# Kernel tuning notes

Measured on AMD Instinct MI355X. Metric: run time of the kernel, lower is better.

Reference implementation:

```python
import jax, jax.numpy as jnp
import numpy as np

NUM_HEADS = 16
HIDDEN = 1024
DIM = HIDDEN // NUM_HEADS  # 64
NEG = -1e8
LN_EPS = 1e-5


def setup_inputs() -> dict:
    key = jax.random.key(0)
    ks = jax.random.split(key, 8)
    B, Lq, Lk = 8, 512, 2048
    s = 0.02
    return {
        "input_embed": jax.random.normal(ks[0], (B, Lq, HIDDEN), jnp.float32),
        "kg_embed": jax.random.normal(ks[1], (B, Lk, HIDDEN), jnp.float32),
        "input_mask": jnp.ones((B, Lq), jnp.float32),
        "kg_mask": jnp.ones((B, Lk), jnp.float32),
        "Wq": jax.random.normal(ks[2], (DIM, DIM), jnp.float32) * s,
        "Wk": jax.random.normal(ks[3], (DIM, DIM), jnp.float32) * s,
        "Wv": jax.random.normal(ks[4], (DIM, DIM), jnp.float32) * s,
        "W_lin": jax.random.normal(ks[5], (HIDDEN, HIDDEN), jnp.float32) * s,
        "b_lin": jnp.zeros((HIDDEN,), jnp.float32),
        "ln_gamma": jnp.ones((HIDDEN,), jnp.float32),
        "ln_beta": jnp.zeros((HIDDEN,), jnp.float32),
    }


def reference(input_embed, kg_embed, input_mask, kg_mask, Wq, Wk, Wv, W_lin, b_lin, ln_gamma, ln_beta):
    B, Lq, H = input_embed.shape
    Lk = kg_embed.shape[1]
    # split heads: per-head slices share the SAME dim x dim q/k/v weights
    xq = input_embed.reshape(B, Lq, NUM_HEADS, DIM)
    xk = kg_embed.reshape(B, Lk, NUM_HEADS, DIM)
    q = jnp.einsum('bqhd,ed->bqhe', xq, Wq)  # Linear: x @ W.T
    k = jnp.einsum('bkhd,ed->bkhe', xk, Wk)
    v = jnp.einsum('bkhd,ed->bkhe', xk, Wv)
    scores = jnp.einsum('bqhd,bkhd->bhqk', q, k) / np.sqrt(DIM)  # [B,H,Lq,Lk]
    # additive masks: query-side and key-side
    scores = scores + ((1.0 - input_mask) * NEG)[:, None, :, None] \
                    + ((1.0 - kg_mask) * NEG)[:, None, None, :]
    attn = jax.nn.softmax(scores, axis=-1)
    ctx = jnp.einsum('bhqk,bkhd->bqhd', attn, v).reshape(B, Lq, H)  # concat heads
    lin = ctx @ W_lin.T + b_lin
    x = jax.nn.gelu(lin, approximate=False) + input_embed  # nn.GELU() is exact erf
    mu = jnp.mean(x, axis=-1, keepdims=True)
    var = jnp.mean(jnp.square(x - mu), axis=-1, keepdims=True)
    return (x - mu) * jax.lax.rsqrt(var + LN_EPS) * ln_gamma + ln_beta
```

## Files before the change

kernel.cpp:

```cpp
#include <hip/hip_runtime.h>
#include <cstdint>

#define BATCH 8
#define LQ 512
#define LK 2048
#define NH 16
#define DIM 64
#define HID 1024
#define NTOK (BATCH * LQ)
#define NKT (LK / 64)
#define KP 72
#define SC 0.1803368801111204f
#define NEGM (-1.4426950408889634e8f)

typedef _Float16 f16x8 __attribute__((ext_vector_type(8)));
typedef __fp16 half2v __attribute__((ext_vector_type(2)));
typedef float f32x4 __attribute__((ext_vector_type(4)));

#define MFMA(a, b, c) __builtin_amdgcn_mfma_f32_16x16x32_f16((a), (b), (c), 0, 0, 0)

__device__ __forceinline__ f16x8 ld8(const _Float16* p) { return *(const f16x8*)p; }

__device__ __forceinline__ void gl_lds16(const void* g, void* l) {
  __builtin_amdgcn_global_load_lds(
      (const __attribute__((address_space(1))) uint32_t*)g,
      (__attribute__((address_space(3))) uint32_t*)l, 16, 0, 0);
}

__device__ __forceinline__ void lds_barrier() {
  asm volatile("s_waitcnt lgkmcnt(0)" ::: "memory");
  __builtin_amdgcn_s_barrier();
}

__device__ __forceinline__ f16x8 cvt8(const float* p) {
  const float4 a = *(const float4*)p;
  const float4 b = *(const float4*)(p + 4);
  f16x8 v;
  v[0] = (_Float16)a.x; v[1] = (_Float16)a.y; v[2] = (_Float16)a.z; v[3] = (_Float16)a.w;
  v[4] = (_Float16)b.x; v[5] = (_Float16)b.y; v[6] = (_Float16)b.z; v[7] = (_Float16)b.w;
  return v;
}

__device__ __forceinline__ uint2 pk4(float a, float b, float c, float d) {
  union { half2v h2[2]; uint2 u; } t;
  t.h2[0] = __builtin_amdgcn_cvt_pkrtz(a, b);
  t.h2[1] = __builtin_amdgcn_cvt_pkrtz(c, d);
  return t.u;
}

__device__ __forceinline__ f16x8 pk8(float4 a, float4 b) {
  union { half2v h2[4]; f16x8 v; } t;
  t.h2[0] = __builtin_amdgcn_cvt_pkrtz(a.x, a.y);
  t.h2[1] = __builtin_amdgcn_cvt_pkrtz(a.z, a.w);
  t.h2[2] = __builtin_amdgcn_cvt_pkrtz(b.x, b.y);
  t.h2[3] = __builtin_amdgcn_cvt_pkrtz(b.z, b.w);
  return t.v;
}

__global__ __launch_bounds__(512, 2) void attn_kernel(
    const float* __restrict__ Xq, const float* __restrict__ Xk,
    const float* __restrict__ Wq, const float* __restrict__ Wk,
    const float* __restrict__ Wv, const float* __restrict__ kg_mask,
    _Float16* __restrict__ ctx) {
  __shared__ __align__(16) _Float16 Kl[2][64 * KP];
  __shared__ __align__(16) _Float16 Vl[2][64 * KP];
  __shared__ __align__(16) _Float16 Pl[8][2][16 * KP];
  const int tid = threadIdx.x;
  const int wave = tid >> 6, lane = tid & 63, l16 = lane & 15, quad = lane >> 4;
  const int kw = wave & 3;
  const int b = blockIdx.x >> 4, h = blockIdx.x & 15;
  const int qbase = blockIdx.y * 256;
  const float* Xg = Xk + (size_t)b * LK * HID + h * 64;
  const float* mg = kg_mask + (size_t)b * LK;

  const float* xrow0 = Xg + (size_t)(kw * 16 + l16) * HID + quad * 8;
  float4 xf0, xf1, xf2, xf3;
  auto loadX = [&](int kt) {
    const float* xr = xrow0 + (size_t)kt * HID;
    xf0 = *(const float4*)(xr);
    xf1 = *(const float4*)(xr + 4);
    xf2 = *(const float4*)(xr + 32);
    xf3 = *(const float4*)(xr + 36);
  };
  loadX(0);

  f16x8 aq0[2], aq1[2];
  {
    f16x8 wq0[4], wq1[4];
#pragma unroll
    for (int nt = 0; nt < 4; ++nt) {
      const float* wp = Wq + (nt * 16 + l16) * DIM + quad * 8;
      wq0[nt] = cvt8(wp);
      wq1[nt] = cvt8(wp + 32);
    }
#pragma unroll
    for (int qt = 0; qt < 2; ++qt) {
      const int qg = qbase + wave * 32 + qt * 16 + l16;
      const float* xpq = Xq + (size_t)(b * LQ + qg) * HID + h * 64 + quad * 8;
      const f16x8 bq0 = cvt8(xpq), bq1 = cvt8(xpq + 32);
#pragma unroll
      for (int nt = 0; nt < 4; ++nt) {
        f32x4 d = {0.f, 0.f, 0.f, 0.f};
        d = MFMA(wq0[nt], bq0, d);
        d = MFMA(wq1[nt], bq1, d);
        *(uint2*)&Pl[wave][qt][l16 * KP + nt * 16 + quad * 4] =
            pk4(d[0] * SC, d[1] * SC, d[2] * SC, d[3] * SC);
      }
      aq0[qt] = ld8(&Pl[wave][qt][l16 * KP + quad * 8]);
      aq1[qt] = ld8(&Pl[wave][qt][l16 * KP + 32 + quad * 8]);
    }
  }

  const float* Wsel = (wave < 4) ? Wk : Wv;
  f16x8 aw0[4], aw1[4];
#pragma unroll
  for (int nt = 0; nt < 4; ++nt) {
    const float* wp = Wsel + (nt * 16 + l16) * DIM + quad * 8;
    aw0[nt] = cvt8(wp);
    aw1[nt] = cvt8(wp + 32);
  }

  const f32x4 z4 = {0.f, 0.f, 0.f, 0.f};

  {
    const f16x8 bx0 = pk8(xf0, xf1), bx1 = pk8(xf2, xf3);
    if (wave < 4) {
#pragma unroll
      for (int nt = 0; nt < 4; ++nt) {
        f32x4 d = z4;
        d = MFMA(aw0[nt], bx0, d);
        d = MFMA(aw1[nt], bx1, d);
        *(uint2*)&Kl[0][(kw * 16 + l16) * KP + nt * 16 + quad * 4] =
            pk4(d[0], d[1], d[2], d[3]);
      }
    } else {
#pragma unroll
      for (int dt = 0; dt < 4; ++dt) {
        f32x4 d = z4;
        d = MFMA(bx0, aw0[dt], d);
        d = MFMA(bx1, aw1[dt], d);
        *(uint2*)&Vl[0][(dt * 16 + l16) * KP + kw * 16 + quad * 4] =
            pk4(d[0], d[1], d[2], d[3]);
      }
    }
  }
  loadX(64);
  lds_barrier();

  f32x4 o[2][4];
  float l_run[2] = {0.f, 0.f};
#pragma unroll
  for (int qt = 0; qt < 2; ++qt)
#pragma unroll
    for (int i = 0; i < 4; ++i) o[qt][i] = z4;

  for (int t = 0; t < NKT; ++t) {
    const int buf = t & 1;
    const int kt = t * 64;

    float4 mq[4];
#pragma unroll
    for (int nt = 0; nt < 4; ++nt)
      mq[nt] = *(const float4*)(mg + kt + nt * 16 + quad * 4);

    if (t + 1 < NKT) {
      const f16x8 bx0 = pk8(xf0, xf1), bx1 = pk8(xf2, xf3);
      if (wave < 4) {
#pragma unroll
        for (int nt = 0; nt < 4; ++nt) {
          f32x4 d = z4;
          d = MFMA(aw0[nt], bx0, d);
          d = MFMA(aw1[nt], bx1, d);
          *(uint2*)&Kl[buf ^ 1][(kw * 16 + l16) * KP + nt * 16 + quad * 4] =
              pk4(d[0], d[1], d[2], d[3]);
        }
      } else {
#pragma unroll
        for (int dt = 0; dt < 4; ++dt) {
          f32x4 d = z4;
          d = MFMA(bx0, aw0[dt], d);
          d = MFMA(bx1, aw1[dt], d);
          *(uint2*)&Vl[buf ^ 1][(dt * 16 + l16) * KP + kw * 16 + quad * 4] =
              pk4(d[0], d[1], d[2], d[3]);
        }
      }
      if (t + 2 < NKT) loadX(kt + 128);
    }

    f32x4 cin[4];
#pragma unroll
    for (int nt = 0; nt < 4; ++nt) {
      cin[nt][0] = __builtin_fmaf(mq[nt].x, -NEGM, NEGM);
      cin[nt][1] = __builtin_fmaf(mq[nt].y, -NEGM, NEGM);
      cin[nt][2] = __builtin_fmaf(mq[nt].z, -NEGM, NEGM);
      cin[nt][3] = __builtin_fmaf(mq[nt].w, -NEGM, NEGM);
    }

    float p[2][4][4];
    __builtin_amdgcn_s_setprio(1);
#pragma unroll
    for (int nt = 0; nt < 4; ++nt) {
      const f16x8 kb0 = ld8(&Kl[buf][(nt * 16 + l16) * KP + quad * 8]);
      const f16x8 kb1 = ld8(&Kl[buf][(nt * 16 + l16) * KP + 32 + quad * 8]);
#pragma unroll
      for (int qt = 0; qt < 2; ++qt) {
        f32x4 s = cin[nt];
        s = MFMA(kb0, aq0[qt], s);
        s = MFMA(kb1, aq1[qt], s);
        const float e0 = __builtin_amdgcn_exp2f(s[0]);
        const float e1 = __builtin_amdgcn_exp2f(s[1]);
        const float e2 = __builtin_amdgcn_exp2f(s[2]);
        const float e3 = __builtin_amdgcn_exp2f(s[3]);
        l_run[qt] += (e0 + e1) + (e2 + e3);
        p[qt][nt][0] = e0; p[qt][nt][1] = e1; p[qt][nt][2] = e2; p[qt][nt][3] = e3;
      }
    }
    __builtin_amdgcn_s_setprio(0);

#pragma unroll
    for (int qt = 0; qt < 2; ++qt)
#pragma unroll
      for (int nt = 0; nt < 4; ++nt)
        *(uint2*)&Pl[wave][qt][l16 * KP + nt * 16 + quad * 4] =
            pk4(p[qt][nt][0], p[qt][nt][1], p[qt][nt][2], p[qt][nt][3]);
    f16x8 ap0[2], ap1[2];
#pragma unroll
    for (int qt = 0; qt < 2; ++qt) {
      ap0[qt] = ld8(&Pl[wave][qt][l16 * KP + quad * 8]);
      ap1[qt] = ld8(&Pl[wave][qt][l16 * KP + 32 + quad * 8]);
    }

    __builtin_amdgcn_s_setprio(1);
#pragma unroll
    for (int dt = 0; dt < 4; ++dt) {
      const f16x8 vb0 = ld8(&Vl[buf][(dt * 16 + l16) * KP + quad * 8]);
      const f16x8 vb1 = ld8(&Vl[buf][(dt * 16 + l16) * KP + 32 + quad * 8]);
#pragma unroll
      for (int qt = 0; qt < 2; ++qt) {
        o[qt][dt] = MFMA(vb0, ap0[qt], o[qt][dt]);
        o[qt][dt] = MFMA(vb1, ap1[qt], o[qt][dt]);
      }
    }
    __builtin_amdgcn_s_setprio(0);

    lds_barrier();
  }

  float inv[2];
#pragma unroll
  for (int qt = 0; qt < 2; ++qt) {
    float s = l_run[qt];
    s += __shfl_xor(s, 16);
    s += __shfl_xor(s, 32);
    inv[qt] = 1.f / s;
  }
#pragma unroll
  for (int qt = 0; qt < 2; ++qt) {
    const int qg = qbase + wave * 32 + qt * 16 + l16;
    _Float16* base = ctx + (size_t)(b * LQ + qg) * HID + h * 64;
#pragma unroll
    for (int dt = 0; dt < 4; ++dt)
      *(uint2*)(base + dt * 16 + quad * 4) =
          pk4(o[qt][dt][0] * inv[qt], o[qt][dt][1] * inv[qt],
              o[qt][dt][2] * inv[qt], o[qt][dt][3] * inv[qt]);
  }
}

__global__ __launch_bounds__(256) void wconv_kernel(const float* __restrict__ W,
                                                    _Float16* __restrict__ Wh) {
  const int i = blockIdx.x * 256 + threadIdx.x;
  const float4 v = ((const float4*)W)[i];
  ((uint2*)Wh)[i] = pk4(v.x, v.y, v.z, v.w);
}

__global__ __launch_bounds__(512) void linear_kernel(const _Float16* __restrict__ A,
                                                     const _Float16* __restrict__ Wh,
                                                     const float* __restrict__ bias,
                                                     const float* __restrict__ resid,
                                                     float* __restrict__ Xout) {
  __shared__ __align__(16) _Float16 Al[2][128 * 64];
  __shared__ __align__(16) _Float16 Bl[2][128 * 64];
  const int tid = threadIdx.x;
  const int wave = tid >> 6, lane = tid & 63, l16 = lane & 15, quad = lane >> 4;
  const int wm = wave >> 2, wn = wave & 3;
  const int nbase = blockIdx.x * 128, mbase = blockIdx.y * 128;
  const int srow = wave * 16 + (lane >> 3);
  const int sc = lane & 7;

  auto stage = [&](int kk, int nbuf) {
#pragma unroll
    for (int i = 0; i < 2; ++i) {
      const int row = srow + i * 8;
      const int c = sc ^ (row & 7);
      gl_lds16(A + (size_t)(mbase + row) * HID + kk + c * 8,
               &Al[nbuf][(wave * 16 + i * 8) * 64]);
      gl_lds16(Wh + (size_t)(nbase + row) * HID + kk + c * 8,
               &Bl[nbuf][(wave * 16 + i * 8) * 64]);
    }
  };

  const f32x4 z4 = {0.f, 0.f, 0.f, 0.f};
  f32x4 acc[4][2];
#pragma unroll
  for (int mt = 0; mt < 4; ++mt)
#pragma unroll
    for (int nt = 0; nt < 2; ++nt) acc[mt][nt] = z4;

  stage(0, 0);
  for (int t = 0; t < HID / 64; ++t) {
    const int buf = t & 1;
    __syncthreads();
    if (t + 1 < HID / 64) stage((t + 1) * 64, buf ^ 1);
    const int sw = l16 & 7;
    f16x8 b0[2], b1[2];
#pragma unroll
    for (int nt = 0; nt < 2; ++nt) {
      const int brow = wn * 32 + nt * 16 + l16;
      b0[nt] = ld8(&Bl[buf][brow * 64 + (quad ^ sw) * 8]);
      b1[nt] = ld8(&Bl[buf][brow * 64 + ((quad + 4) ^ sw) * 8]);
    }
#pragma unroll
    for (int mt = 0; mt < 4; ++mt) {
      const int arow = wm * 64 + mt * 16 + l16;
      const f16x8 a0 = ld8(&Al[buf][arow * 64 + (quad ^ sw) * 8]);
      const f16x8 a1 = ld8(&Al[buf][arow * 64 + ((quad + 4) ^ sw) * 8]);
#pragma unroll
      for (int nt = 0; nt < 2; ++nt) {
        acc[mt][nt] = MFMA(a0, b0[nt], acc[mt][nt]);
        acc[mt][nt] = MFMA(a1, b1[nt], acc[mt][nt]);
      }
    }
  }
#pragma unroll
  for (int nt = 0; nt < 2; ++nt) {
    const int col = nbase + wn * 32 + nt * 16 + l16;
    const float bv = bias[col];
#pragma unroll
    for (int mt = 0; mt < 4; ++mt) {
#pragma unroll
      for (int r = 0; r < 4; ++r) {
        const int row = mbase + wm * 64 + mt * 16 + quad * 4 + r;
        const float v = acc[mt][nt][r] + bv;
        const float g = 0.5f * v * (1.f + erff(v * 0.70710678118654752f));
        Xout[(size_t)row * HID + col] = g + resid[(size_t)row * HID + col];
      }
    }
  }
}

__global__ __launch_bounds__(256) void ln_kernel(const float* __restrict__ X,
                                                 const float* __restrict__ gamma,
                                                 const float* __restrict__ beta,
                                                 float* __restrict__ out) {
  const int row = blockIdx.x, tid = threadIdx.x;
  const int lane = tid & 63, wave = tid >> 6;
  const float4 v = *(const float4*)(X + (size_t)row * HID + tid * 4);
  float s1 = v.x + v.y + v.z + v.w;
  float s2 = v.x * v.x + v.y * v.y + v.z * v.z + v.w * v.w;
#pragma unroll
  for (int off = 1; off < 64; off <<= 1) {
    s1 += __shfl_xor(s1, off);
    s2 += __shfl_xor(s2, off);
  }
  __shared__ float r1[4], r2[4];
  if (lane == 0) { r1[wave] = s1; r2[wave] = s2; }
  __syncthreads();
  s1 = r1[0] + r1[1] + r1[2] + r1[3];
  s2 = r2[0] + r2[1] + r2[2] + r2[3];
  const float mu = s1 * (1.f / HID);
  const float var = s2 * (1.f / HID) - mu * mu;
  const float rstd = rsqrtf(var + 1e-5f);
  const float4 g = *(const float4*)(gamma + tid * 4);
  const float4 be = *(const float4*)(beta + tid * 4);
  float4 ov;
  ov.x = (v.x - mu) * rstd * g.x + be.x;
  ov.y = (v.y - mu) * rstd * g.y + be.y;
  ov.z = (v.z - mu) * rstd * g.z + be.z;
  ov.w = (v.w - mu) * rstd * g.w + be.w;
  *(float4*)(out + (size_t)row * HID + tid * 4) = ov;
}

extern "C" void kernel_launch(void* const* d_in, const int* in_sizes, int n_in,
                              void* d_out, int out_size, void* d_ws, size_t ws_size,
                              hipStream_t stream) {
  (void)in_sizes; (void)n_in; (void)out_size; (void)ws_size;
  const float* input_embed = (const float*)d_in[0];
  const float* kg_embed    = (const float*)d_in[1];
  const float* kg_mask = (const float*)d_in[3];
  const float* Wq    = (const float*)d_in[4];
  const float* Wk    = (const float*)d_in[5];
  const float* Wv    = (const float*)d_in[6];
  const float* W_lin = (const float*)d_in[7];
  const float* b_lin = (const float*)d_in[8];
  const float* gamma = (const float*)d_in[9];
  const float* beta  = (const float*)d_in[10];

  char* ws = (char*)d_ws;
  _Float16* ctx = (_Float16*)(ws);
  float*    Xb  = (float*)(ws + (8u << 20));
  _Float16* Wh  = (_Float16*)(ws + (24u << 20));

  attn_kernel<<<dim3(128, 2), dim3(512), 0, stream>>>(input_embed, kg_embed, Wq, Wk, Wv,
                                                      kg_mask, ctx);
  wconv_kernel<<<dim3(1024), dim3(256), 0, stream>>>(W_lin, Wh);
  linear_kernel<<<dim3(8, 32), dim3(512), 0, stream>>>(ctx, Wh, b_lin, input_embed, Xb);
  ln_kernel<<<dim3(NTOK), dim3(256), 0, stream>>>(Xb, gamma, beta, (float*)d_out);
}
```

Measured before the change: 210.7 us.

## Split attention over key dimension with partial outputs and combine kernel

Splits the key/value sequence into two halves across a new grid z dimension, so the attention kernel launches twice as many blocks. Each split writes unnormalized fp32 partial outputs and row sums, and a new combine kernel sums them, normalizes and emits fp16 context. This works without max-rescaling because the softmax has no running max. The aim is to fill the MI355X's CUs better than the original 256-block grid did. The cost is recomputing the Q projection per split, extra global traffic for the fp32 partials, and one more kernel launch. It also shrinks the P scratch LDS buffer to one tile per wave.

```diff
diff --git a/kernel.cpp b/kernel.cpp
--- a/kernel.cpp
+++ b/kernel.cpp
@@ -57,19 +57,23 @@
   return t.v;
 }
 
+template <int NZ>
 __global__ __launch_bounds__(512, 2) void attn_kernel(
     const float* __restrict__ Xq, const float* __restrict__ Xk,
     const float* __restrict__ Wq, const float* __restrict__ Wk,
     const float* __restrict__ Wv, const float* __restrict__ kg_mask,
-    _Float16* __restrict__ ctx) {
+    _Float16* __restrict__ ctx, float* __restrict__ Opart,
+    float* __restrict__ lpart) {
   __shared__ __align__(16) _Float16 Kl[2][64 * KP];
   __shared__ __align__(16) _Float16 Vl[2][64 * KP];
-  __shared__ __align__(16) _Float16 Pl[8][2][16 * KP];
+  __shared__ __align__(16) _Float16 Pl[8][16 * KP];
   const int tid = threadIdx.x;
   const int wave = tid >> 6, lane = tid & 63, l16 = lane & 15, quad = lane >> 4;
   const int kw = wave & 3;
   const int b = blockIdx.x >> 4, h = blockIdx.x & 15;
   const int qbase = blockIdx.y * 256;
+  const int kz = blockIdx.z * (LK / NZ);
+  const int NT = NKT / NZ;
   const float* Xg = Xk + (size_t)b * LK * HID + h * 64;
   const float* mg = kg_mask + (size_t)b * LK;
 
@@ -82,7 +86,7 @@
     xf2 = *(const float4*)(xr + 32);
     xf3 = *(const float4*)(xr + 36);
   };
-  loadX(0);
+  loadX(kz);
 
   f16x8 aq0[2], aq1[2];
   {
@@ -103,11 +107,11 @@
         f32x4 d = {0.f, 0.f, 0.f, 0.f};
         d = MFMA(wq0[nt], bq0, d);
         d = MFMA(wq1[nt], bq1, d);
-        *(uint2*)&Pl[wave][qt][l16 * KP + nt * 16 + quad * 4] =
+        *(uint2*)&Pl[wave][l16 * KP + nt * 16 + quad * 4] =
             pk4(d[0] * SC, d[1] * SC, d[2] * SC, d[3] * SC);
       }
-      aq0[qt] = ld8(&Pl[wave][qt][l16 * KP + quad * 8]);
-      aq1[qt] = ld8(&Pl[wave][qt][l16 * KP + 32 + quad * 8]);
+      aq0[qt] = ld8(&Pl[wave][l16 * KP + quad * 8]);
+      aq1[qt] = ld8(&Pl[wave][l16 * KP + 32 + quad * 8]);
     }
   }
 
@@ -144,7 +148,7 @@
       }
     }
   }
-  loadX(64);
+  loadX(kz + 64);
   lds_barrier();
 
   f32x4 o[2][4];
@@ -154,16 +158,16 @@
 #pragma unroll
     for (int i = 0; i < 4; ++i) o[qt][i] = z4;
 
-  for (int t = 0; t < NKT; ++t) {
+  for (int t = 0; t < NT; ++t) {
     const int buf = t & 1;
-    const int kt = t * 64;
+    const int kt = kz + t * 64;
 
     float4 mq[4];
 #pragma unroll
     for (int nt = 0; nt < 4; ++nt)
       mq[nt] = *(const float4*)(mg + kt + nt * 16 + quad * 4);
 
-    if (t + 1 < NKT) {
+    if (t + 1 < NT) {
       const f16x8 bx0 = pk8(xf0, xf1), bx1 = pk8(xf2, xf3);
       if (wave < 4) {
 #pragma unroll
@@ -184,7 +188,7 @@
               pk4(d[0], d[1], d[2], d[3]);
         }
       }
-      if (t + 2 < NKT) loadX(kt + 128);
+      if (t + 2 < NT) loadX(kt + 128);
     }
 
     f32x4 cin[4];
@@ -217,17 +221,15 @@
     }
     __builtin_amdgcn_s_setprio(0);
 
-#pragma unroll
-    for (int qt = 0; qt < 2; ++qt)
+    f16x8 ap0[2], ap1[2];
+#pragma unroll
+    for (int qt = 0; qt < 2; ++qt) {
 #pragma unroll
       for (int nt = 0; nt < 4; ++nt)
-        *(uint2*)&Pl[wave][qt][l16 * KP + nt * 16 + quad * 4] =
+        *(uint2*)&Pl[wave][l16 * KP + nt * 16 + quad * 4] =
             pk4(p[qt][nt][0], p[qt][nt][1], p[qt][nt][2], p[qt][nt][3]);
-    f16x8 ap0[2], ap1[2];
-#pragma unroll
-    for (int qt = 0; qt < 2; ++qt) {
-      ap0[qt] = ld8(&Pl[wave][qt][l16 * KP + quad * 8]);
-      ap1[qt] = ld8(&Pl[wave][qt][l16 * KP + 32 + quad * 8]);
+      ap0[qt] = ld8(&Pl[wave][l16 * KP + quad * 8]);
+      ap1[qt] = ld8(&Pl[wave][l16 * KP + 32 + quad * 8]);
     }
 
     __builtin_amdgcn_s_setprio(1);
@@ -246,24 +248,50 @@
     lds_barrier();
   }
 
-  float inv[2];
 #pragma unroll
   for (int qt = 0; qt < 2; ++qt) {
     float s = l_run[qt];
     s += __shfl_xor(s, 16);
     s += __shfl_xor(s, 32);
-    inv[qt] = 1.f / s;
-  }
-#pragma unroll
-  for (int qt = 0; qt < 2; ++qt) {
     const int qg = qbase + wave * 32 + qt * 16 + l16;
-    _Float16* base = ctx + (size_t)(b * LQ + qg) * HID + h * 64;
-#pragma unroll
-    for (int dt = 0; dt < 4; ++dt)
-      *(uint2*)(base + dt * 16 + quad * 4) =
-          pk4(o[qt][dt][0] * inv[qt], o[qt][dt][1] * inv[qt],
-              o[qt][dt][2] * inv[qt], o[qt][dt][3] * inv[qt]);
-  }
+    if constexpr (NZ == 1) {
+      const float inv = 1.f / s;
+      _Float16* base = ctx + (size_t)(b * LQ + qg) * HID + h * 64;
+#pragma unroll
+      for (int dt = 0; dt < 4; ++dt)
+        *(uint2*)(base + dt * 16 + quad * 4) =
+            pk4(o[qt][dt][0] * inv, o[qt][dt][1] * inv,
+                o[qt][dt][2] * inv, o[qt][dt][3] * inv);
+    } else {
+      if (quad == 0)
+        lpart[((size_t)(blockIdx.z * BATCH + b) * NH + h) * LQ + qg] = s;
+      float* obase = Opart + (size_t)blockIdx.z * NTOK * HID +
+                     (size_t)(b * LQ + qg) * HID + h * 64;
+#pragma unroll
+      for (int dt = 0; dt < 4; ++dt) {
+        float4 ov;
+        ov.x = o[qt][dt][0]; ov.y = o[qt][dt][1];
+        ov.z = o[qt][dt][2]; ov.w = o[qt][dt][3];
+        *(float4*)(obase + dt * 16 + quad * 4) = ov;
+      }
+    }
+  }
+}
+
+__global__ __launch_bounds__(256) void combine_kernel(
+    const float* __restrict__ Opart, const float* __restrict__ lpart,
+    _Float16* __restrict__ ctx) {
+  const int tok = blockIdx.x, t = threadIdx.x;
+  const int b = tok >> 9, q = tok & 511;
+  const int hh = t >> 4;
+  const float l0 = lpart[((size_t)b * NH + hh) * LQ + q];
+  const float l1 = lpart[((size_t)(BATCH + b) * NH + hh) * LQ + q];
+  const float inv = 1.f / (l0 + l1);
+  const size_t off = (size_t)tok * HID + t * 4;
+  const float4 a = *(const float4*)(Opart + off);
+  const float4 c = *(const float4*)(Opart + (size_t)NTOK * HID + off);
+  *(uint2*)(ctx + off) = pk4((a.x + c.x) * inv, (a.y + c.y) * inv,
+                             (a.z + c.z) * inv, (a.w + c.w) * inv);
 }
 
 __global__ __launch_bounds__(256) void wconv_kernel(const float* __restrict__ W,
@@ -383,7 +411,7 @@
 extern "C" void kernel_launch(void* const* d_in, const int* in_sizes, int n_in,
                               void* d_out, int out_size, void* d_ws, size_t ws_size,
                               hipStream_t stream) {
-  (void)in_sizes; (void)n_in; (void)out_size; (void)ws_size;
+  (void)in_sizes; (void)n_in; (void)out_size;
   const float* input_embed = (const float*)d_in[0];
   const float* kg_embed    = (const float*)d_in[1];
   const float* kg_mask = (const float*)d_in[3];
@@ -399,9 +427,17 @@
   _Float16* ctx = (_Float16*)(ws);
   float*    Xb  = (float*)(ws + (8u << 20));
   _Float16* Wh  = (_Float16*)(ws + (24u << 20));
-
-  attn_kernel<<<dim3(128, 2), dim3(512), 0, stream>>>(input_embed, kg_embed, Wq, Wk, Wv,
-                                                      kg_mask, ctx);
+  float* Opart  = (float*)(ws + (26u << 20));
+  float* lpart  = (float*)(ws + (58u << 20));
+
+  if (ws_size >= (59ull << 20)) {
+    attn_kernel<2><<<dim3(128, 2, 2), dim3(512), 0, stream>>>(
+        input_embed, kg_embed, Wq, Wk, Wv, kg_mask, ctx, Opart, lpart);
+    combine_kernel<<<dim3(NTOK), dim3(256), 0, stream>>>(Opart, lpart, ctx);
+  } else {
+    attn_kernel<1><<<dim3(128, 2, 1), dim3(512), 0, stream>>>(
+        input_embed, kg_embed, Wq, Wk, Wv, kg_mask, ctx, Opart, lpart);
+  }
   wconv_kernel<<<dim3(1024), dim3(256), 0, stream>>>(W_lin, Wh);
   linear_kernel<<<dim3(8, 32), dim3(512), 0, stream>>>(ctx, Wh, b_lin, input_embed, Xb);
   ln_kernel<<<dim3(NTOK), dim3(256), 0, stream>>>(Xb, gamma, beta, (float*)d_out);
```

New measurement: 229.7 us. +9.0%, slower.

## Switch attention to 32x32x16 MFMA and pass P via permlane32 swap

Applied to the files above, without the earlier changes.

Rewrites the attention inner loop to use 32x32x16 f16 MFMA tiles instead of 16x16x32, giving each wave a single 32-query tile with 32x32 score and output accumulators. The probability matrix is re-laid out into the B-operand format in registers with permlane32_swap, replacing the LDS store and reload through Pl. This is meant to cut LDS traffic and MFMA instruction count per tile. In exchange it uses more accumulator registers and changes the mask and output indexing, which risks register pressure and occupancy at 2 blocks per CU.

```diff
diff --git a/kernel.cpp b/kernel.cpp
--- a/kernel.cpp
+++ b/kernel.cpp
@@ -16,8 +16,11 @@
 typedef _Float16 f16x8 __attribute__((ext_vector_type(8)));
 typedef __fp16 half2v __attribute__((ext_vector_type(2)));
 typedef float f32x4 __attribute__((ext_vector_type(4)));
+typedef float f32x16 __attribute__((ext_vector_type(16)));
+typedef unsigned uint2v __attribute__((ext_vector_type(2)));
 
 #define MFMA(a, b, c) __builtin_amdgcn_mfma_f32_16x16x32_f16((a), (b), (c), 0, 0, 0)
+#define MFMA32(a, b, c) __builtin_amdgcn_mfma_f32_32x32x16_f16((a), (b), (c), 0, 0, 0)
 
 __device__ __forceinline__ f16x8 ld8(const _Float16* p) { return *(const f16x8*)p; }
 
@@ -45,6 +48,12 @@
   union { half2v h2[2]; uint2 u; } t;
   t.h2[0] = __builtin_amdgcn_cvt_pkrtz(a, b);
   t.h2[1] = __builtin_amdgcn_cvt_pkrtz(c, d);
+  return t.u;
+}
+
+__device__ __forceinline__ uint32_t pk2(float a, float b) {
+  union { half2v h2; uint32_t u; } t;
+  t.h2 = __builtin_amdgcn_cvt_pkrtz(a, b);
   return t.u;
 }
 
@@ -68,6 +77,9 @@
   const int tid = threadIdx.x;
   const int wave = tid >> 6, lane = tid & 63, l16 = lane & 15, quad = lane >> 4;
   const int kw = wave & 3;
+  const int ql = lane & 31;
+  const int kh = (lane >> 5) * 8;
+  const int khm = (lane >> 5) * 4;
   const int b = blockIdx.x >> 4, h = blockIdx.x & 15;
   const int qbase = blockIdx.y * 256;
   const float* Xg = Xk + (size_t)b * LK * HID + h * 64;
@@ -84,7 +96,7 @@
   };
   loadX(0);
 
-  f16x8 aq0[2], aq1[2];
+  f16x8 q32[4];
   {
     f16x8 wq0[4], wq1[4];
 #pragma unroll
@@ -106,9 +118,11 @@
         *(uint2*)&Pl[wave][qt][l16 * KP + nt * 16 + quad * 4] =
             pk4(d[0] * SC, d[1] * SC, d[2] * SC, d[3] * SC);
       }
-      aq0[qt] = ld8(&Pl[wave][qt][l16 * KP + quad * 8]);
-      aq1[qt] = ld8(&Pl[wave][qt][l16 * KP + 32 + quad * 8]);
-    }
+    }
+    const int qt2 = ql >> 4, qr = ql & 15;
+#pragma unroll
+    for (int es = 0; es < 4; ++es)
+      q32[es] = ld8(&Pl[wave][qt2][qr * KP + es * 16 + kh]);
   }
 
   const float* Wsel = (wave < 4) ? Wk : Wv;
@@ -147,21 +161,21 @@
   loadX(64);
   lds_barrier();
 
-  f32x4 o[2][4];
-  float l_run[2] = {0.f, 0.f};
-#pragma unroll
-  for (int qt = 0; qt < 2; ++qt)
-#pragma unroll
-    for (int i = 0; i < 4; ++i) o[qt][i] = z4;
+  f32x16 og[2];
+#pragma unroll
+  for (int i = 0; i < 16; ++i) { og[0][i] = 0.f; og[1][i] = 0.f; }
+  float l_run = 0.f;
 
   for (int t = 0; t < NKT; ++t) {
     const int buf = t & 1;
     const int kt = t * 64;
 
-    float4 mq[4];
-#pragma unroll
-    for (int nt = 0; nt < 4; ++nt)
-      mq[nt] = *(const float4*)(mg + kt + nt * 16 + quad * 4);
+    float4 mraw[2][4];
+#pragma unroll
+    for (int g = 0; g < 2; ++g)
+#pragma unroll
+      for (int c = 0; c < 4; ++c)
+        mraw[g][c] = *(const float4*)(mg + kt + g * 32 + c * 8 + khm);
 
     if (t + 1 < NKT) {
       const f16x8 bx0 = pk8(xf0, xf1), bx1 = pk8(xf2, xf3);
@@ -187,82 +201,87 @@
       if (t + 2 < NKT) loadX(kt + 128);
     }
 
-    f32x4 cin[4];
-#pragma unroll
-    for (int nt = 0; nt < 4; ++nt) {
-      cin[nt][0] = __builtin_fmaf(mq[nt].x, -NEGM, NEGM);
-      cin[nt][1] = __builtin_fmaf(mq[nt].y, -NEGM, NEGM);
-      cin[nt][2] = __builtin_fmaf(mq[nt].z, -NEGM, NEGM);
-      cin[nt][3] = __builtin_fmaf(mq[nt].w, -NEGM, NEGM);
-    }
-
-    float p[2][4][4];
+    f16x8 vb[2][4];
+#pragma unroll
+    for (int dg = 0; dg < 2; ++dg)
+#pragma unroll
+      for (int ks = 0; ks < 4; ++ks)
+        vb[dg][ks] = ld8(&Vl[buf][(dg * 32 + ql) * KP + ks * 16 + kh]);
+
+    f32x16 cin[2];
+#pragma unroll
+    for (int g = 0; g < 2; ++g)
+#pragma unroll
+      for (int c = 0; c < 4; ++c) {
+        cin[g][c * 4 + 0] = __builtin_fmaf(mraw[g][c].x, -NEGM, NEGM);
+        cin[g][c * 4 + 1] = __builtin_fmaf(mraw[g][c].y, -NEGM, NEGM);
+        cin[g][c * 4 + 2] = __builtin_fmaf(mraw[g][c].z, -NEGM, NEGM);
+        cin[g][c * 4 + 3] = __builtin_fmaf(mraw[g][c].w, -NEGM, NEGM);
+      }
+
+    float p[2][16];
+    float t0 = 0.f, t1 = 0.f, t2 = 0.f, t3 = 0.f;
     __builtin_amdgcn_s_setprio(1);
 #pragma unroll
-    for (int nt = 0; nt < 4; ++nt) {
-      const f16x8 kb0 = ld8(&Kl[buf][(nt * 16 + l16) * KP + quad * 8]);
-      const f16x8 kb1 = ld8(&Kl[buf][(nt * 16 + l16) * KP + 32 + quad * 8]);
-#pragma unroll
-      for (int qt = 0; qt < 2; ++qt) {
-        f32x4 s = cin[nt];
-        s = MFMA(kb0, aq0[qt], s);
-        s = MFMA(kb1, aq1[qt], s);
-        const float e0 = __builtin_amdgcn_exp2f(s[0]);
-        const float e1 = __builtin_amdgcn_exp2f(s[1]);
-        const float e2 = __builtin_amdgcn_exp2f(s[2]);
-        const float e3 = __builtin_amdgcn_exp2f(s[3]);
-        l_run[qt] += (e0 + e1) + (e2 + e3);
-        p[qt][nt][0] = e0; p[qt][nt][1] = e1; p[qt][nt][2] = e2; p[qt][nt][3] = e3;
+    for (int g = 0; g < 2; ++g) {
+      f32x16 s = cin[g];
+#pragma unroll
+      for (int es = 0; es < 4; ++es) {
+        const f16x8 kf = ld8(&Kl[buf][(g * 32 + ql) * KP + es * 16 + kh]);
+        s = MFMA32(kf, q32[es], s);
+      }
+#pragma unroll
+      for (int c = 0; c < 4; ++c) {
+        const float e0 = __builtin_amdgcn_exp2f(s[c * 4 + 0]);
+        const float e1 = __builtin_amdgcn_exp2f(s[c * 4 + 1]);
+        const float e2 = __builtin_amdgcn_exp2f(s[c * 4 + 2]);
+        const float e3 = __builtin_amdgcn_exp2f(s[c * 4 + 3]);
+        p[g][c * 4 + 0] = e0; p[g][c * 4 + 1] = e1;
+        p[g][c * 4 + 2] = e2; p[g][c * 4 + 3] = e3;
+        t0 += e0; t1 += e1; t2 += e2; t3 += e3;
       }
     }
     __builtin_amdgcn_s_setprio(0);
-
-#pragma unroll
-    for (int qt = 0; qt < 2; ++qt)
-#pragma unroll
-      for (int nt = 0; nt < 4; ++nt)
-        *(uint2*)&Pl[wave][qt][l16 * KP + nt * 16 + quad * 4] =
-            pk4(p[qt][nt][0], p[qt][nt][1], p[qt][nt][2], p[qt][nt][3]);
-    f16x8 ap0[2], ap1[2];
-#pragma unroll
-    for (int qt = 0; qt < 2; ++qt) {
-      ap0[qt] = ld8(&Pl[wave][qt][l16 * KP + quad * 8]);
-      ap1[qt] = ld8(&Pl[wave][qt][l16 * KP + 32 + quad * 8]);
+    l_run += (t0 + t1) + (t2 + t3);
+
+    f16x8 pf[4];
+#pragma unroll
+    for (int ks = 0; ks < 4; ++ks) {
+      const int g = ks >> 1, base = (ks & 1) * 8;
+      const uint32_t a0 = pk2(p[g][base + 0], p[g][base + 1]);
+      const uint32_t b0 = pk2(p[g][base + 4], p[g][base + 5]);
+      const uint32_t a1 = pk2(p[g][base + 2], p[g][base + 3]);
+      const uint32_t b1 = pk2(p[g][base + 6], p[g][base + 7]);
+      const uint2v r0 = __builtin_amdgcn_permlane32_swap(a0, b0, false, false);
+      const uint2v r1 = __builtin_amdgcn_permlane32_swap(a1, b1, false, false);
+      union { uint32_t u[4]; f16x8 v; } tt;
+      tt.u[0] = r0.x; tt.u[1] = r1.x; tt.u[2] = r0.y; tt.u[3] = r1.y;
+      pf[ks] = tt.v;
     }
 
     __builtin_amdgcn_s_setprio(1);
 #pragma unroll
-    for (int dt = 0; dt < 4; ++dt) {
-      const f16x8 vb0 = ld8(&Vl[buf][(dt * 16 + l16) * KP + quad * 8]);
-      const f16x8 vb1 = ld8(&Vl[buf][(dt * 16 + l16) * KP + 32 + quad * 8]);
-#pragma unroll
-      for (int qt = 0; qt < 2; ++qt) {
-        o[qt][dt] = MFMA(vb0, ap0[qt], o[qt][dt]);
-        o[qt][dt] = MFMA(vb1, ap1[qt], o[qt][dt]);
-      }
-    }
+    for (int dg = 0; dg < 2; ++dg)
+#pragma unroll
+      for (int ks = 0; ks < 4; ++ks)
+        og[dg] = MFMA32(vb[dg][ks], pf[ks], og[dg]);
     __builtin_amdgcn_s_setprio(0);
 
     lds_barrier();
   }
 
-  float inv[2];
-#pragma unroll
-  for (int qt = 0; qt < 2; ++qt) {
-    float s = l_run[qt];
-    s += __shfl_xor(s, 16);
-    s += __shfl_xor(s, 32);
-    inv[qt] = 1.f / s;
-  }
-#pragma unroll
-  for (int qt = 0; qt < 2; ++qt) {
-    const int qg = qbase + wave * 32 + qt * 16 + l16;
+  const float lsum = l_run + __shfl_xor(l_run, 32);
+  const float inv = 1.f / lsum;
+  {
+    const int qg = qbase + wave * 32 + ql;
     _Float16* base = ctx + (size_t)(b * LQ + qg) * HID + h * 64;
 #pragma unroll
-    for (int dt = 0; dt < 4; ++dt)
-      *(uint2*)(base + dt * 16 + quad * 4) =
-          pk4(o[qt][dt][0] * inv[qt], o[qt][dt][1] * inv[qt],
-              o[qt][dt][2] * inv[qt], o[qt][dt][3] * inv[qt]);
+    for (int dg = 0; dg < 2; ++dg)
+#pragma unroll
+      for (int c = 0; c < 4; ++c)
+        *(uint2*)(base + dg * 32 + c * 8 + khm) =
+            pk4(og[dg][c * 4 + 0] * inv, og[dg][c * 4 + 1] * inv,
+                og[dg][c * 4 + 2] * inv, og[dg][c * 4 + 3] * inv);
   }
 }
 
```

New measurement: 224.8 us. 6.7% more time.
